# Kernel optimization log

Hardware: AMD Instinct MI355X
Metric: run time of the kernel (lower is better)

The kernel has to match this reference:

```python
import jax, jax.numpy as jnp
import numpy as np

LAYERS, STACKS = 10, 4
DILATIONS = [2 ** l for _ in range(STACKS) for l in range(LAYERS)]  # 40 blocks


def setup_inputs() -> dict:
    key = jax.random.key(0)
    ks = jax.random.split(key, 7)
    B, C, L, SC, NB = 4, 64, 8192, 256, len(DILATIONS)
    scale = 0.05  # keep 40 stacked residual blocks numerically tame
    return {
        "x": jax.random.normal(ks[0], (B, C, L), dtype=jnp.float32),
        "dc_w": jax.random.normal(ks[1], (NB, C, C, 2), dtype=jnp.float32) * scale,
        "dc_b": jax.random.normal(ks[2], (NB, C), dtype=jnp.float32) * scale,
        "conv_w": jax.random.normal(ks[3], (NB, C, C), dtype=jnp.float32) * scale,
        "conv_b": jax.random.normal(ks[4], (NB, C), dtype=jnp.float32) * scale,
        "skip_w": jax.random.normal(ks[5], (NB, SC, C), dtype=jnp.float32) * scale,
        "skip_b": jax.random.normal(ks[6], (NB, SC), dtype=jnp.float32) * scale,
        "skip_size": 4096,
    }


def reference(x, dc_w, dc_b, conv_w, conv_b, skip_w, skip_b, skip_size):
    # x: [B, res_ch, L]; returns stacked skips [n_blocks, B, skip_ch, skip_size]
    out = x
    skips = []
    for i, d in enumerate(DILATIONS):
        h = (jnp.einsum('oi,bil->bol', dc_w[i, :, :, 0], out[:, :, :-d])
             + jnp.einsum('oi,bil->bol', dc_w[i, :, :, 1], out[:, :, d:])
             + dc_b[i][None, :, None])
        g = jax.nn.relu(h)
        r = jnp.einsum('oi,bil->bol', conv_w[i], g) + conv_b[i][None, :, None]
        out = r + out[:, :, -r.shape[2]:]  # residual on aligned (last) timesteps
        s = jnp.einsum('oi,bil->bol', skip_w[i], g) + skip_b[i][None, :, None]
        skips.append(s[:, :, -skip_size:])
    return jnp.stack(skips)
```

## Files before the change

kernel.cpp:

```cpp
#include <hip/hip_runtime.h>


#define CC    64
#define SCC   256
#define BB    4
#define LL0   8192
#define NBLK  40
#define SKIPN 4096
#define TTC   32
#define STT   64

typedef __attribute__((ext_vector_type(8))) short bf16x8;
typedef __attribute__((ext_vector_type(4))) float f32x4;

__device__ __forceinline__ unsigned short f2bf(float f) {
    union { float f; unsigned u; } v; v.f = f;
    return (unsigned short)((v.u + 0x7FFF + ((v.u >> 16) & 1)) >> 16);
}

__global__ __launch_bounds__(256) void prep_weights(
    const float* __restrict__ dc_w, const float* __restrict__ conv_w,
    const float* __restrict__ skip_w,
    unsigned short* __restrict__ wcat,
    unsigned short* __restrict__ cwb,
    unsigned short* __restrict__ swb)
{
    const int n_sw = NBLK * SCC * CC;
    const int n_cw = NBLK * CC * CC;
    const int n_wc = NBLK * CC * 128;
    for (int idx = blockIdx.x * blockDim.x + threadIdx.x; idx < n_sw;
         idx += gridDim.x * blockDim.x) {
        swb[idx] = f2bf(skip_w[idx]);
        if (idx < n_cw) cwb[idx] = f2bf(conv_w[idx]);
        if (idx < n_wc) {
            const int i = idx >> 13, o = (idx >> 7) & 63, kk = idx & 127;
            wcat[idx] = f2bf(dc_w[(((i * CC + o) * CC) + (kk & 63)) * 2 + (kk >> 6)]);
        }
    }
}

__device__ __forceinline__ void skip_body(
    int id, const unsigned short* __restrict__ g,
    const unsigned short* __restrict__ sw, const float* __restrict__ sb,
    float* __restrict__ op)
{
    const int tid = threadIdx.x, lane = tid & 63, wv = tid >> 6;
    const int tt = id & 63;
    const int b  = id >> 6;
    const unsigned short* gb = g + (size_t)b * SKIPN * CC;
    float* ob = op + (size_t)b * SCC * SKIPN;

    const int trow = tt * STT + wv * 16 + (lane & 15);
    bf16x8 a[2];
    #pragma unroll
    for (int ks = 0; ks < 2; ++ks)
        a[ks] = *(const bf16x8*)(gb + (size_t)trow * CC + ks * 32 + (lane >> 4) * 8);

    const int tstore = tt * STT + wv * 16 + ((lane >> 4) << 2);
    #pragma unroll 4
    for (int n = 0; n < 16; ++n) {
        const int sc = n * 16 + (lane & 15);
        const float bias = sb[sc];
        f32x4 acc = (f32x4){bias, bias, bias, bias};
        const unsigned short* wrow = sw + sc * CC + (lane >> 4) * 8;
        acc = __builtin_amdgcn_mfma_f32_16x16x32_bf16(a[0], *(const bf16x8*)(wrow), acc, 0, 0, 0);
        acc = __builtin_amdgcn_mfma_f32_16x16x32_bf16(a[1], *(const bf16x8*)(wrow + 32), acc, 0, 0, 0);
        *(float4*)(ob + (size_t)sc * SKIPN + tstore) = (float4){acc[0], acc[1], acc[2], acc[3]};
    }
}

__global__ __launch_bounds__(256) void block_kernel(
    const float* __restrict__ cur, float* __restrict__ nxt,
    const unsigned short* __restrict__ wcat, const unsigned short* __restrict__ cwb,
    const float* __restrict__ db, const float* __restrict__ cb,
    unsigned short* __restrict__ g_out,
    int d, int Lin, int Lout, int ntiles,
    const unsigned short* __restrict__ g_prev,
    const unsigned short* __restrict__ swb_prev,
    const float* __restrict__ sb_prev,
    float* __restrict__ out_prev)
{
    const int wg = blockIdx.x;
    const int chain_wgs = BB * ntiles;
    if (wg >= chain_wgs) {
        skip_body(wg - chain_wgs, g_prev, swb_prev, sb_prev, out_prev);
        return;
    }

    __shared__ __align__(16) unsigned short xt[TTC * 128];
    __shared__ __align__(16) unsigned short gs[TTC * CC];
    __shared__ float x1f[CC][TTC + 1];

    const int tid = threadIdx.x, lane = tid & 63, wv = tid >> 6;
    const int b  = wg / ntiles;
    const int t0 = (wg % ntiles) * TTC;
    const float* src = cur + (size_t)b * CC * LL0;

    {
        const int c  = (tid & 31) * 2;
        const int tg = tid >> 5;
        const bool full = (t0 + TTC + d <= Lin);
        #pragma unroll
        for (int op = 0; op < 2; ++op) {
            const int doff = op ? d : 0;
            const int tb = t0 + tg * 4 + doff;
            float v0[4], v1[4];
            if (full && (op == 0 || (d & 3) == 0)) {
                *(float4*)v0 = *(const float4*)(src + (size_t)c * LL0 + tb);
                *(float4*)v1 = *(const float4*)(src + (size_t)(c + 1) * LL0 + tb);
            } else {
                #pragma unroll
                for (int j = 0; j < 4; ++j) {
                    int t = tb + j; if (t > Lin - 1) t = Lin - 1;
                    v0[j] = src[(size_t)c * LL0 + t];
                    v1[j] = src[(size_t)(c + 1) * LL0 + t];
                }
            }
            const int kk = op * 64 + c;
            const int chunk = kk >> 3, sub = kk & 7;
            #pragma unroll
            for (int j = 0; j < 4; ++j) {
                const int row = tg * 4 + j;
                const unsigned pack = (unsigned)f2bf(v0[j]) | ((unsigned)f2bf(v1[j]) << 16);
                *(unsigned*)((char*)xt + row * 256 + ((chunk ^ (row & 7)) * 16) + sub * 2) = pack;
            }
            if (op == 1) {
                #pragma unroll
                for (int j = 0; j < 4; ++j) {
                    x1f[c][tg * 4 + j]     = v0[j];
                    x1f[c + 1][tg * 4 + j] = v1[j];
                }
            }
        }
    }
    __syncthreads();

    const int rf = wv >> 1;
    const int oh = wv & 1;

    bf16x8 a1[4];
    {
        const int row = rf * 16 + (lane & 15);
        #pragma unroll
        for (int ks = 0; ks < 4; ++ks) {
            const int chunk = ks * 4 + (lane >> 4);
            a1[ks] = *(const bf16x8*)((const char*)xt + row * 256 + ((chunk ^ (row & 7)) * 16));
        }
    }
    f32x4 acc[2];
    #pragma unroll
    for (int n = 0; n < 2; ++n) {
        const int o = oh * 32 + n * 16 + (lane & 15);
        const float bias = db[o];
        acc[n] = (f32x4){bias, bias, bias, bias};
        const unsigned short* wrow = wcat + o * 128 + (lane >> 4) * 8;
        #pragma unroll
        for (int ks = 0; ks < 4; ++ks)
            acc[n] = __builtin_amdgcn_mfma_f32_16x16x32_bf16(
                a1[ks], *(const bf16x8*)(wrow + ks * 32), acc[n], 0, 0, 0);
    }
    {
        const int trow0 = rf * 16 + ((lane >> 4) << 2);
        #pragma unroll
        for (int n = 0; n < 2; ++n) {
            const int o = oh * 32 + n * 16 + (lane & 15);
            const int chunkb = o >> 3, sub = o & 7;
            #pragma unroll
            for (int r = 0; r < 4; ++r) {
                float g = acc[n][r]; g = g > 0.f ? g : 0.f;
                const int row = trow0 + r;
                *(unsigned short*)((char*)gs + row * 128 + ((chunkb ^ (row & 7)) * 16) + sub * 2) = f2bf(g);
            }
        }
    }
    __syncthreads();

    bf16x8 a2[2];
    {
        const int row = rf * 16 + (lane & 15);
        #pragma unroll
        for (int ks = 0; ks < 2; ++ks) {
            const int chunk = ks * 4 + (lane >> 4);
            a2[ks] = *(const bf16x8*)((const char*)gs + row * 128 + ((chunk ^ (row & 7)) * 16));
        }
    }
    {
        const int tloc = rf * 16 + ((lane >> 4) << 2);
        const int t = t0 + tloc;
        #pragma unroll
        for (int n = 0; n < 2; ++n) {
            const int o = oh * 32 + n * 16 + (lane & 15);
            const float bias = cb[o];
            f32x4 racc = (f32x4){bias, bias, bias, bias};
            const unsigned short* wrow = cwb + o * 64 + (lane >> 4) * 8;
            racc = __builtin_amdgcn_mfma_f32_16x16x32_bf16(a2[0], *(const bf16x8*)(wrow), racc, 0, 0, 0);
            racc = __builtin_amdgcn_mfma_f32_16x16x32_bf16(a2[1], *(const bf16x8*)(wrow + 32), racc, 0, 0, 0);
            float* outp = nxt + (size_t)b * CC * LL0 + (size_t)o * LL0 + t;
            if (t + 3 < Lout) {
                *(float4*)outp = (float4){racc[0] + x1f[o][tloc + 0],
                                          racc[1] + x1f[o][tloc + 1],
                                          racc[2] + x1f[o][tloc + 2],
                                          racc[3] + x1f[o][tloc + 3]};
            } else {
                #pragma unroll
                for (int r = 0; r < 4; ++r)
                    if (t + r < Lout) outp[r] = racc[r] + x1f[o][tloc + r];
            }
        }
    }

    {
        const int skip_start = Lout - SKIPN;
        const int row = tid >> 3;
        const int ch  = tid & 7;
        const int t = t0 + row;
        if (t >= skip_start && t < Lout) {
            unsigned short* gr = g_out + ((size_t)b * SKIPN + (t - skip_start)) * CC;
            bf16x8 vv = *(const bf16x8*)((const char*)gs + row * 128 + ((ch ^ (row & 7)) * 16));
            *(bf16x8*)(gr + ch * 8) = vv;
        }
    }
}

__global__ __launch_bounds__(256) void skip_kernel(
    const unsigned short* __restrict__ g, const unsigned short* __restrict__ sw,
    const float* __restrict__ sb, float* __restrict__ op)
{
    skip_body(blockIdx.x, g, sw, sb, op);
}

extern "C" void kernel_launch(void* const* d_in, const int* in_sizes, int n_in,
                              void* d_out, int out_size, void* d_ws, size_t ws_size,
                              hipStream_t stream)
{
    const float* x      = (const float*)d_in[0];
    const float* dc_w   = (const float*)d_in[1];
    const float* dc_b   = (const float*)d_in[2];
    const float* conv_w = (const float*)d_in[3];
    const float* conv_b = (const float*)d_in[4];
    const float* skip_w = (const float*)d_in[5];
    const float* skip_b = (const float*)d_in[6];
    float* out = (float*)d_out;

    char* ws = (char*)d_ws;
    float* buf0 = (float*)ws;                    ws += (size_t)BB * CC * LL0 * 4;
    float* buf1 = (float*)ws;                    ws += (size_t)BB * CC * LL0 * 4;
    unsigned short* g_all = (unsigned short*)ws; ws += (size_t)NBLK * BB * SKIPN * CC * 2;
    unsigned short* wcat  = (unsigned short*)ws; ws += (size_t)NBLK * CC * 128 * 2;
    unsigned short* cwb   = (unsigned short*)ws; ws += (size_t)NBLK * CC * CC * 2;
    unsigned short* swb   = (unsigned short*)ws; ws += (size_t)NBLK * SCC * CC * 2;

    prep_weights<<<1024, 256, 0, stream>>>(dc_w, conv_w, skip_w, wcat, cwb, swb);

    const int skip_wgs = BB * (SKIPN / STT);
    int Lc = LL0;
    for (int i = 0; i < NBLK; ++i) {
        const int d = 1 << (i % 10);
        const int Lout = Lc - d;
        const int ntiles = (Lout + TTC - 1) / TTC;
        const float* curp = (i == 0) ? x : ((i & 1) ? buf0 : buf1);
        float*       nxtp = (i & 1) ? buf1 : buf0;
        const int j = i - 1;
        const int grid = BB * ntiles + (i ? skip_wgs : 0);
        block_kernel<<<dim3(grid), 256, 0, stream>>>(
            curp, nxtp,
            wcat + (size_t)i * CC * 128, cwb + (size_t)i * CC * CC,
            dc_b + i * CC, conv_b + i * CC,
            g_all + (size_t)i * BB * SKIPN * CC,
            d, Lc, Lout, ntiles,
            g_all + (size_t)(i ? j : 0) * BB * SKIPN * CC,
            swb + (size_t)(i ? j : 0) * SCC * CC,
            skip_b + (i ? j : 0) * SCC,
            out + (size_t)(i ? j : 0) * BB * SCC * SKIPN);
        Lc = Lout;
    }
    skip_kernel<<<dim3(skip_wgs), 256, 0, stream>>>(
        g_all + (size_t)(NBLK - 1) * BB * SKIPN * CC,
        swb + (size_t)(NBLK - 1) * SCC * CC,
        skip_b + (NBLK - 1) * SCC,
        out + (size_t)(NBLK - 1) * BB * SCC * SKIPN);
}
```

Before: 853.1 us.

## Fuse small-dilation WaveNet blocks in shared memory with time-major activation layout

Activations switch from channel-major to time-major layout through a new transpose kernel. The first six blocks of each stack (dilations 1 to 32) now run in one fused kernel that keeps a haloed tile in LDS across all six layers, so the residual stream does not make global round-trips between them. The skip GEMMs for all six fused blocks overlap with the next launch. This cuts launches and global traffic for the residual stream. In exchange it recomputes the halo rows and uses larger LDS footprints with 512-thread blocks, which may reduce occupancy.

Measured after the change: 742.6 us. 1.15x faster.

```diff
diff --git a/kernel.cpp b/kernel.cpp
--- a/kernel.cpp
+++ b/kernel.cpp
@@ -8,7 +8,6 @@
 #define NBLK  40
 #define SKIPN 4096
 #define TTC   32
-#define STT   64
 
 typedef __attribute__((ext_vector_type(8))) short bf16x8;
 typedef __attribute__((ext_vector_type(4))) float f32x4;
@@ -16,6 +15,25 @@
 __device__ __forceinline__ unsigned short f2bf(float f) {
     union { float f; unsigned u; } v; v.f = f;
     return (unsigned short)((v.u + 0x7FFF + ((v.u >> 16) & 1)) >> 16);
+}
+__device__ __forceinline__ bf16x8 pack8(f32x4 u0, f32x4 u1) {
+    bf16x8 r;
+    r[0] = (short)f2bf(u0[0]); r[1] = (short)f2bf(u0[1]);
+    r[2] = (short)f2bf(u0[2]); r[3] = (short)f2bf(u0[3]);
+    r[4] = (short)f2bf(u1[0]); r[5] = (short)f2bf(u1[1]);
+    r[6] = (short)f2bf(u1[2]); r[7] = (short)f2bf(u1[3]);
+    return r;
+}
+__device__ __forceinline__ int sws(int row, int c) {
+    return (row << 6) + (((((c >> 3) ^ row) & 7) << 3) | (c & 7));
+}
+__device__ __forceinline__ int swg(int row, int o) {
+    return (row << 6) + (((((o >> 3) ^ row) & 7) << 3) | (o & 7));
+}
+__device__ __forceinline__ int swx(int row, int kk) {
+    int ch = kk >> 3;
+    ch = (ch & 8) | ((ch ^ row) & 7);
+    return (row << 7) + (ch << 3) + (kk & 7);
 }
 
 __global__ __launch_bounds__(256) void prep_weights(
@@ -39,24 +57,55 @@
     }
 }
 
+__global__ __launch_bounds__(256) void transpose_x(
+    const float* __restrict__ x, float* __restrict__ dst)
+{
+    __shared__ float tile[64][65];
+    const int b = blockIdx.y, t0 = blockIdx.x * 64;
+    const int tid = threadIdx.x;
+    #pragma unroll
+    for (int p = 0; p < 4; ++p) {
+        const int c = p * 16 + (tid >> 4);
+        const int j = tid & 15;
+        const float4 v = *(const float4*)(x + ((size_t)b * CC + c) * LL0 + t0 + j * 4);
+        tile[c][j * 4 + 0] = v.x; tile[c][j * 4 + 1] = v.y;
+        tile[c][j * 4 + 2] = v.z; tile[c][j * 4 + 3] = v.w;
+    }
+    __syncthreads();
+    #pragma unroll
+    for (int p = 0; p < 4; ++p) {
+        const int r = p * 16 + (tid >> 4);
+        const int h = tid & 15;
+        float4 v = {tile[h * 4 + 0][r], tile[h * 4 + 1][r],
+                    tile[h * 4 + 2][r], tile[h * 4 + 3][r]};
+        *(float4*)(dst + ((size_t)b * LL0 + t0 + r) * CC + h * 4) = v;
+    }
+}
+
+template<int NW>
 __device__ __forceinline__ void skip_body(
-    int id, const unsigned short* __restrict__ g,
-    const unsigned short* __restrict__ sw, const float* __restrict__ sb,
-    float* __restrict__ op)
-{
+    int e, int prev_blk0,
+    const unsigned short* __restrict__ g_all,
+    const unsigned short* __restrict__ swb,
+    const float* __restrict__ skip_b, float* __restrict__ out)
+{
+    constexpr int ROWS = NW * 16;
+    constexpr int TPB = (SKIPN / ROWS) * BB;
     const int tid = threadIdx.x, lane = tid & 63, wv = tid >> 6;
-    const int tt = id & 63;
-    const int b  = id >> 6;
-    const unsigned short* gb = g + (size_t)b * SKIPN * CC;
-    float* ob = op + (size_t)b * SCC * SKIPN;
-
-    const int trow = tt * STT + wv * 16 + (lane & 15);
+    const int j = prev_blk0 + e / TPB;
+    const int id = e % TPB;
+    const int tt = id % (SKIPN / ROWS);
+    const int b  = id / (SKIPN / ROWS);
+    const unsigned short* g = g_all + ((size_t)j * BB + b) * SKIPN * CC;
+    const unsigned short* sw = swb + (size_t)j * SCC * CC;
+    const float* sb = skip_b + j * SCC;
+    float* op = out + ((size_t)j * BB + b) * SCC * SKIPN;
+
+    const int trow = tt * ROWS + wv * 16 + (lane & 15);
     bf16x8 a[2];
-    #pragma unroll
-    for (int ks = 0; ks < 2; ++ks)
-        a[ks] = *(const bf16x8*)(gb + (size_t)trow * CC + ks * 32 + (lane >> 4) * 8);
-
-    const int tstore = tt * STT + wv * 16 + ((lane >> 4) << 2);
+    a[0] = *(const bf16x8*)(g + (size_t)trow * CC + (lane >> 4) * 8);
+    a[1] = *(const bf16x8*)(g + (size_t)trow * CC + 32 + (lane >> 4) * 8);
+    const int tstore = tt * ROWS + wv * 16 + ((lane >> 4) << 2);
     #pragma unroll 4
     for (int n = 0; n < 16; ++n) {
         const int sc = n * 16 + (lane & 15);
@@ -65,7 +114,171 @@
         const unsigned short* wrow = sw + sc * CC + (lane >> 4) * 8;
         acc = __builtin_amdgcn_mfma_f32_16x16x32_bf16(a[0], *(const bf16x8*)(wrow), acc, 0, 0, 0);
         acc = __builtin_amdgcn_mfma_f32_16x16x32_bf16(a[1], *(const bf16x8*)(wrow + 32), acc, 0, 0, 0);
-        *(float4*)(ob + (size_t)sc * SKIPN + tstore) = (float4){acc[0], acc[1], acc[2], acc[3]};
+        *(float4*)(op + (size_t)sc * SKIPN + tstore) = (float4){acc[0], acc[1], acc[2], acc[3]};
+    }
+}
+
+template<int NB, int DB, int TOUT, int R0CAP, int GSCAP, int MAXCH>
+__global__ __launch_bounds__(512) void fused_kernel(
+    const float* __restrict__ cur, float* __restrict__ nxt,
+    const unsigned short* __restrict__ wcat_all, const unsigned short* __restrict__ cwb_all,
+    const float* __restrict__ db_all, const float* __restrict__ cb_all,
+    unsigned short* __restrict__ g_all, int blk0, int Lin, int ntiles,
+    const unsigned short* __restrict__ swb, const float* __restrict__ skip_b,
+    float* __restrict__ out, int prev_blk0, int prev_nblk)
+{
+    const int wg = blockIdx.x;
+    const int chain = BB * ntiles;
+    if (wg >= chain) {
+        skip_body<8>(wg - chain, prev_blk0, g_all, swb, skip_b, out);
+        return;
+    }
+
+    constexpr int H  = DB * ((1 << NB) - 1);
+    constexpr int R0 = TOUT + H;
+    __shared__ __align__(16) float sm[R0CAP * CC];
+    __shared__ __align__(16) unsigned short gsm[GSCAP * CC];
+
+    const int tid = threadIdx.x, lane = tid & 63, wv = tid >> 6;
+    const int b = wg / ntiles, t0 = (wg % ntiles) * TOUT;
+    const float* src = cur + (size_t)b * LL0 * CC;
+
+    for (int base = 0; base < R0; base += 32) {
+        const int row = base + (tid >> 4);
+        const int h = tid & 15;
+        if (row < R0) {
+            int gt = t0 + row; if (gt > Lin - 1) gt = Lin - 1;
+            *(f32x4*)(sm + sws(row, h * 4)) =
+                *(const f32x4*)(src + (size_t)gt * CC + h * 4);
+        }
+    }
+    __syncthreads();
+
+    const int rf = wv >> 1, oh = wv & 1;
+    int Rcur = R0, Lj = Lin;
+
+    for (int j = 0; j < NB; ++j) {
+        const int d = DB << j;
+        const int Rn = Rcur - d;
+        Lj -= d;
+        const unsigned short* wj  = wcat_all + (size_t)(blk0 + j) * CC * 128;
+        const unsigned short* cj  = cwb_all + (size_t)(blk0 + j) * CC * CC;
+        const float* dbj = db_all + (blk0 + j) * CC;
+        const float* cbj = cb_all + (blk0 + j) * CC;
+
+        #pragma unroll
+        for (int ch = 0; ch < MAXCH; ++ch) {
+            if (ch * 64 < Rn) {
+                int row = ch * 64 + rf * 16 + (lane & 15);
+                if (row > Rn - 1) row = Rn - 1;
+                bf16x8 a1[4];
+                #pragma unroll
+                for (int ks = 0; ks < 2; ++ks) {
+                    const int c0 = ks * 32 + (lane >> 4) * 8;
+                    a1[ks] = pack8(*(const f32x4*)(sm + sws(row, c0)),
+                                   *(const f32x4*)(sm + sws(row, c0 + 4)));
+                    a1[2 + ks] = pack8(*(const f32x4*)(sm + sws(row + d, c0)),
+                                       *(const f32x4*)(sm + sws(row + d, c0 + 4)));
+                }
+                f32x4 acc[2];
+                #pragma unroll
+                for (int n = 0; n < 2; ++n) {
+                    const int o = oh * 32 + n * 16 + (lane & 15);
+                    const float bias = dbj[o];
+                    acc[n] = (f32x4){bias, bias, bias, bias};
+                    const unsigned short* wrow = wj + o * 128 + (lane >> 4) * 8;
+                    #pragma unroll
+                    for (int ks = 0; ks < 4; ++ks)
+                        acc[n] = __builtin_amdgcn_mfma_f32_16x16x32_bf16(
+                            a1[ks], *(const bf16x8*)(wrow + ks * 32), acc[n], 0, 0, 0);
+                }
+                const int wr = ch * 64 + rf * 16 + ((lane >> 4) << 2);
+                #pragma unroll
+                for (int n = 0; n < 2; ++n) {
+                    const int o = oh * 32 + n * 16 + (lane & 15);
+                    #pragma unroll
+                    for (int r = 0; r < 4; ++r) {
+                        const int rr = wr + r;
+                        if (rr < Rn) {
+                            float g = acc[n][r]; g = g > 0.f ? g : 0.f;
+                            gsm[swg(rr, o)] = f2bf(g);
+                        }
+                    }
+                }
+            }
+        }
+        __syncthreads();
+
+        f32x4 racc[MAXCH][2];
+        f32x4 oldv[MAXCH][2];
+        #pragma unroll
+        for (int ch = 0; ch < MAXCH; ++ch) {
+            if (ch * 64 < Rn) {
+                int row = ch * 64 + rf * 16 + (lane & 15);
+                if (row > Rn - 1) row = Rn - 1;
+                bf16x8 a2[2];
+                #pragma unroll
+                for (int ks = 0; ks < 2; ++ks)
+                    a2[ks] = *(const bf16x8*)(gsm + swg(row, ks * 32 + (lane >> 4) * 8));
+                const int wr = ch * 64 + rf * 16 + ((lane >> 4) << 2);
+                #pragma unroll
+                for (int n = 0; n < 2; ++n) {
+                    const int o = oh * 32 + n * 16 + (lane & 15);
+                    const float bias = cbj[o];
+                    racc[ch][n] = (f32x4){bias, bias, bias, bias};
+                    const unsigned short* wrow = cj + o * CC + (lane >> 4) * 8;
+                    racc[ch][n] = __builtin_amdgcn_mfma_f32_16x16x32_bf16(
+                        a2[0], *(const bf16x8*)(wrow), racc[ch][n], 0, 0, 0);
+                    racc[ch][n] = __builtin_amdgcn_mfma_f32_16x16x32_bf16(
+                        a2[1], *(const bf16x8*)(wrow + 32), racc[ch][n], 0, 0, 0);
+                    #pragma unroll
+                    for (int r = 0; r < 4; ++r) {
+                        int rr = wr + r; if (rr > Rn - 1) rr = Rn - 1;
+                        oldv[ch][n][r] = sm[sws(rr + d, o)];
+                    }
+                }
+            }
+        }
+        __syncthreads();
+
+        #pragma unroll
+        for (int ch = 0; ch < MAXCH; ++ch) {
+            if (ch * 64 < Rn) {
+                const int wr = ch * 64 + rf * 16 + ((lane >> 4) << 2);
+                #pragma unroll
+                for (int n = 0; n < 2; ++n) {
+                    const int o = oh * 32 + n * 16 + (lane & 15);
+                    #pragma unroll
+                    for (int r = 0; r < 4; ++r) {
+                        const int rr = wr + r;
+                        if (rr < Rn) sm[sws(rr, o)] = racc[ch][n][r] + oldv[ch][n][r];
+                    }
+                }
+            }
+        }
+        {
+            const int wbase = Lj - SKIPN;
+            unsigned short* gdst = g_all + ((size_t)(blk0 + j) * BB + b) * SKIPN * CC;
+            const int ch8 = tid & 7;
+            for (int grow = tid >> 3; grow < Rn; grow += 64) {
+                const int gt = t0 + grow;
+                if (gt < Lj && gt >= wbase)
+                    *(bf16x8*)(gdst + ((size_t)(gt - wbase)) * CC + ch8 * 8) =
+                        *(const bf16x8*)(gsm + (grow << 6) + (((ch8 ^ grow) & 7) << 3));
+            }
+        }
+        __syncthreads();
+        Rcur = Rn;
+    }
+
+    float* dst = nxt + (size_t)b * LL0 * CC;
+    for (int base = 0; base < TOUT; base += 32) {
+        const int row = base + (tid >> 4);
+        const int h = tid & 15;
+        const int gt = t0 + row;
+        if (row < TOUT && gt < Lj)
+            *(float4*)(dst + (size_t)gt * CC + h * 4) =
+                *(const float4*)(sm + sws(row, h * 4));
     }
 }
 
@@ -75,78 +288,55 @@
     const float* __restrict__ db, const float* __restrict__ cb,
     unsigned short* __restrict__ g_out,
     int d, int Lin, int Lout, int ntiles,
-    const unsigned short* __restrict__ g_prev,
-    const unsigned short* __restrict__ swb_prev,
-    const float* __restrict__ sb_prev,
-    float* __restrict__ out_prev)
+    const unsigned short* __restrict__ g_all, const unsigned short* __restrict__ swb,
+    const float* __restrict__ skip_b, float* __restrict__ out,
+    int prev_blk0, int prev_nblk)
 {
     const int wg = blockIdx.x;
-    const int chain_wgs = BB * ntiles;
-    if (wg >= chain_wgs) {
-        skip_body(wg - chain_wgs, g_prev, swb_prev, sb_prev, out_prev);
+    const int chain = BB * ntiles;
+    if (wg >= chain) {
+        skip_body<4>(wg - chain, prev_blk0, g_all, swb, skip_b, out);
         return;
     }
 
     __shared__ __align__(16) unsigned short xt[TTC * 128];
     __shared__ __align__(16) unsigned short gs[TTC * CC];
     __shared__ float x1f[CC][TTC + 1];
+    __shared__ __align__(16) float rs[TTC * CC];
 
     const int tid = threadIdx.x, lane = tid & 63, wv = tid >> 6;
-    const int b  = wg / ntiles;
-    const int t0 = (wg % ntiles) * TTC;
-    const float* src = cur + (size_t)b * CC * LL0;
-
-    {
-        const int c  = (tid & 31) * 2;
-        const int tg = tid >> 5;
-        const bool full = (t0 + TTC + d <= Lin);
-        #pragma unroll
-        for (int op = 0; op < 2; ++op) {
-            const int doff = op ? d : 0;
-            const int tb = t0 + tg * 4 + doff;
-            float v0[4], v1[4];
-            if (full && (op == 0 || (d & 3) == 0)) {
-                *(float4*)v0 = *(const float4*)(src + (size_t)c * LL0 + tb);
-                *(float4*)v1 = *(const float4*)(src + (size_t)(c + 1) * LL0 + tb);
-            } else {
-                #pragma unroll
-                for (int j = 0; j < 4; ++j) {
-                    int t = tb + j; if (t > Lin - 1) t = Lin - 1;
-                    v0[j] = src[(size_t)c * LL0 + t];
-                    v1[j] = src[(size_t)(c + 1) * LL0 + t];
-                }
-            }
-            const int kk = op * 64 + c;
-            const int chunk = kk >> 3, sub = kk & 7;
-            #pragma unroll
-            for (int j = 0; j < 4; ++j) {
-                const int row = tg * 4 + j;
-                const unsigned pack = (unsigned)f2bf(v0[j]) | ((unsigned)f2bf(v1[j]) << 16);
-                *(unsigned*)((char*)xt + row * 256 + ((chunk ^ (row & 7)) * 16) + sub * 2) = pack;
-            }
-            if (op == 1) {
-                #pragma unroll
-                for (int j = 0; j < 4; ++j) {
-                    x1f[c][tg * 4 + j]     = v0[j];
-                    x1f[c + 1][tg * 4 + j] = v1[j];
-                }
-            }
-        }
+    const int b = wg / ntiles, t0 = (wg % ntiles) * TTC;
+    const float* src = cur + (size_t)b * LL0 * CC;
+
+    #pragma unroll
+    for (int p = 0; p < 2; ++p) {
+        const int row = p * 16 + (tid >> 4);
+        const int h = tid & 15;
+        int ta = t0 + row;     if (ta > Lin - 1) ta = Lin - 1;
+        int tb = t0 + row + d; if (tb > Lin - 1) tb = Lin - 1;
+        const float4 v0 = *(const float4*)(src + (size_t)ta * CC + h * 4);
+        const float4 v1 = *(const float4*)(src + (size_t)tb * CC + h * 4);
+        uint2 p0, p1;
+        p0.x = (unsigned)f2bf(v0.x) | ((unsigned)f2bf(v0.y) << 16);
+        p0.y = (unsigned)f2bf(v0.z) | ((unsigned)f2bf(v0.w) << 16);
+        p1.x = (unsigned)f2bf(v1.x) | ((unsigned)f2bf(v1.y) << 16);
+        p1.y = (unsigned)f2bf(v1.z) | ((unsigned)f2bf(v1.w) << 16);
+        *(uint2*)(xt + swx(row, h * 4)) = p0;
+        *(uint2*)(xt + swx(row, 64 + h * 4)) = p1;
+        x1f[h * 4 + 0][row] = v1.x;
+        x1f[h * 4 + 1][row] = v1.y;
+        x1f[h * 4 + 2][row] = v1.z;
+        x1f[h * 4 + 3][row] = v1.w;
     }
     __syncthreads();
 
-    const int rf = wv >> 1;
-    const int oh = wv & 1;
+    const int rf = wv >> 1, oh = wv & 1;
+    const int row = rf * 16 + (lane & 15);
 
     bf16x8 a1[4];
-    {
-        const int row = rf * 16 + (lane & 15);
-        #pragma unroll
-        for (int ks = 0; ks < 4; ++ks) {
-            const int chunk = ks * 4 + (lane >> 4);
-            a1[ks] = *(const bf16x8*)((const char*)xt + row * 256 + ((chunk ^ (row & 7)) * 16));
-        }
-    }
+    #pragma unroll
+    for (int ks = 0; ks < 4; ++ks)
+        a1[ks] = *(const bf16x8*)(xt + swx(row, ks * 32 + (lane >> 4) * 8));
     f32x4 acc[2];
     #pragma unroll
     for (int n = 0; n < 2; ++n) {
@@ -159,74 +349,60 @@
             acc[n] = __builtin_amdgcn_mfma_f32_16x16x32_bf16(
                 a1[ks], *(const bf16x8*)(wrow + ks * 32), acc[n], 0, 0, 0);
     }
+    const int wr = rf * 16 + ((lane >> 4) << 2);
+    #pragma unroll
+    for (int n = 0; n < 2; ++n) {
+        const int o = oh * 32 + n * 16 + (lane & 15);
+        #pragma unroll
+        for (int r = 0; r < 4; ++r) {
+            float g = acc[n][r]; g = g > 0.f ? g : 0.f;
+            gs[swg(wr + r, o)] = f2bf(g);
+        }
+    }
+    __syncthreads();
+
+    bf16x8 a2[2];
+    #pragma unroll
+    for (int ks = 0; ks < 2; ++ks)
+        a2[ks] = *(const bf16x8*)(gs + swg(row, ks * 32 + (lane >> 4) * 8));
+    #pragma unroll
+    for (int n = 0; n < 2; ++n) {
+        const int o = oh * 32 + n * 16 + (lane & 15);
+        const float bias = cb[o];
+        f32x4 racc = (f32x4){bias, bias, bias, bias};
+        const unsigned short* wrow = cwb + o * CC + (lane >> 4) * 8;
+        racc = __builtin_amdgcn_mfma_f32_16x16x32_bf16(a2[0], *(const bf16x8*)(wrow), racc, 0, 0, 0);
+        racc = __builtin_amdgcn_mfma_f32_16x16x32_bf16(a2[1], *(const bf16x8*)(wrow + 32), racc, 0, 0, 0);
+        #pragma unroll
+        for (int r = 0; r < 4; ++r)
+            rs[sws(wr + r, o)] = racc[r] + x1f[o][wr + r];
+    }
+    __syncthreads();
+
+    #pragma unroll
+    for (int p = 0; p < 2; ++p) {
+        const int row2 = p * 16 + (tid >> 4);
+        const int h = tid & 15;
+        const int t = t0 + row2;
+        if (t < Lout)
+            *(float4*)(nxt + (size_t)b * LL0 * CC + (size_t)t * CC + h * 4) =
+                *(const float4*)(rs + sws(row2, h * 4));
+    }
     {
-        const int trow0 = rf * 16 + ((lane >> 4) << 2);
-        #pragma unroll
-        for (int n = 0; n < 2; ++n) {
-            const int o = oh * 32 + n * 16 + (lane & 15);
-            const int chunkb = o >> 3, sub = o & 7;
-            #pragma unroll
-            for (int r = 0; r < 4; ++r) {
-                float g = acc[n][r]; g = g > 0.f ? g : 0.f;
-                const int row = trow0 + r;
-                *(unsigned short*)((char*)gs + row * 128 + ((chunkb ^ (row & 7)) * 16) + sub * 2) = f2bf(g);
-            }
-        }
-    }
-    __syncthreads();
-
-    bf16x8 a2[2];
-    {
-        const int row = rf * 16 + (lane & 15);
-        #pragma unroll
-        for (int ks = 0; ks < 2; ++ks) {
-            const int chunk = ks * 4 + (lane >> 4);
-            a2[ks] = *(const bf16x8*)((const char*)gs + row * 128 + ((chunk ^ (row & 7)) * 16));
-        }
-    }
-    {
-        const int tloc = rf * 16 + ((lane >> 4) << 2);
-        const int t = t0 + tloc;
-        #pragma unroll
-        for (int n = 0; n < 2; ++n) {
-            const int o = oh * 32 + n * 16 + (lane & 15);
-            const float bias = cb[o];
-            f32x4 racc = (f32x4){bias, bias, bias, bias};
-            const unsigned short* wrow = cwb + o * 64 + (lane >> 4) * 8;
-            racc = __builtin_amdgcn_mfma_f32_16x16x32_bf16(a2[0], *(const bf16x8*)(wrow), racc, 0, 0, 0);
-            racc = __builtin_amdgcn_mfma_f32_16x16x32_bf16(a2[1], *(const bf16x8*)(wrow + 32), racc, 0, 0, 0);
-            float* outp = nxt + (size_t)b * CC * LL0 + (size_t)o * LL0 + t;
-            if (t + 3 < Lout) {
-                *(float4*)outp = (float4){racc[0] + x1f[o][tloc + 0],
-                                          racc[1] + x1f[o][tloc + 1],
-                                          racc[2] + x1f[o][tloc + 2],
-                                          racc[3] + x1f[o][tloc + 3]};
-            } else {
-                #pragma unroll
-                for (int r = 0; r < 4; ++r)
-                    if (t + r < Lout) outp[r] = racc[r] + x1f[o][tloc + r];
-            }
-        }
-    }
-
-    {
-        const int skip_start = Lout - SKIPN;
-        const int row = tid >> 3;
-        const int ch  = tid & 7;
-        const int t = t0 + row;
-        if (t >= skip_start && t < Lout) {
-            unsigned short* gr = g_out + ((size_t)b * SKIPN + (t - skip_start)) * CC;
-            bf16x8 vv = *(const bf16x8*)((const char*)gs + row * 128 + ((ch ^ (row & 7)) * 16));
-            *(bf16x8*)(gr + ch * 8) = vv;
-        }
+        const int row2 = tid >> 3, ch8 = tid & 7;
+        const int t = t0 + row2;
+        const int wbase = Lout - SKIPN;
+        if (t >= wbase && t < Lout)
+            *(bf16x8*)(g_out + ((size_t)b * SKIPN + (t - wbase)) * CC + ch8 * 8) =
+                *(const bf16x8*)(gs + (row2 << 6) + (((ch8 ^ row2) & 7) << 3));
     }
 }
 
 __global__ __launch_bounds__(256) void skip_kernel(
-    const unsigned short* __restrict__ g, const unsigned short* __restrict__ sw,
-    const float* __restrict__ sb, float* __restrict__ op)
-{
-    skip_body(blockIdx.x, g, sw, sb, op);
+    const unsigned short* __restrict__ g_all, const unsigned short* __restrict__ swb,
+    const float* __restrict__ skip_b, float* __restrict__ out, int blk)
+{
+    skip_body<4>(blockIdx.x, blk, g_all, swb, skip_b, out);
 }
 
 extern "C" void kernel_launch(void* const* d_in, const int* in_sizes, int n_in,
@@ -243,40 +419,43 @@
     float* out = (float*)d_out;
 
     char* ws = (char*)d_ws;
-    float* buf0 = (float*)ws;                    ws += (size_t)BB * CC * LL0 * 4;
-    float* buf1 = (float*)ws;                    ws += (size_t)BB * CC * LL0 * 4;
+    float* bufA = (float*)ws;                    ws += (size_t)BB * LL0 * CC * 4;
+    float* bufB = (float*)ws;                    ws += (size_t)BB * LL0 * CC * 4;
     unsigned short* g_all = (unsigned short*)ws; ws += (size_t)NBLK * BB * SKIPN * CC * 2;
     unsigned short* wcat  = (unsigned short*)ws; ws += (size_t)NBLK * CC * 128 * 2;
     unsigned short* cwb   = (unsigned short*)ws; ws += (size_t)NBLK * CC * CC * 2;
     unsigned short* swb   = (unsigned short*)ws; ws += (size_t)NBLK * SCC * CC * 2;
 
     prep_weights<<<1024, 256, 0, stream>>>(dc_w, conv_w, skip_w, wcat, cwb, swb);
-
-    const int skip_wgs = BB * (SKIPN / STT);
-    int Lc = LL0;
-    for (int i = 0; i < NBLK; ++i) {
-        const int d = 1 << (i % 10);
-        const int Lout = Lc - d;
-        const int ntiles = (Lout + TTC - 1) / TTC;
-        const float* curp = (i == 0) ? x : ((i & 1) ? buf0 : buf1);
-        float*       nxtp = (i & 1) ? buf1 : buf0;
-        const int j = i - 1;
-        const int grid = BB * ntiles + (i ? skip_wgs : 0);
-        block_kernel<<<dim3(grid), 256, 0, stream>>>(
-            curp, nxtp,
-            wcat + (size_t)i * CC * 128, cwb + (size_t)i * CC * CC,
-            dc_b + i * CC, conv_b + i * CC,
-            g_all + (size_t)i * BB * SKIPN * CC,
-            d, Lc, Lout, ntiles,
-            g_all + (size_t)(i ? j : 0) * BB * SKIPN * CC,
-            swb + (size_t)(i ? j : 0) * SCC * CC,
-            skip_b + (i ? j : 0) * SCC,
-            out + (size_t)(i ? j : 0) * BB * SCC * SKIPN);
-        Lc = Lout;
-    }
-    skip_kernel<<<dim3(skip_wgs), 256, 0, stream>>>(
-        g_all + (size_t)(NBLK - 1) * BB * SKIPN * CC,
-        swb + (size_t)(NBLK - 1) * SCC * CC,
-        skip_b + (NBLK - 1) * SCC,
-        out + (size_t)(NBLK - 1) * BB * SCC * SKIPN);
-}
+    transpose_x<<<dim3(LL0 / 64, BB), 256, 0, stream>>>(x, bufA);
+
+    float* bufs[2] = {bufA, bufB};
+    int Lc = LL0, blk = 0, q = 0, pb0 = 0, pnb = 0;
+    for (int s = 0; s < 4; ++s) {
+        {
+            const int Lout = Lc - 63;
+            const int nt = (Lout + 95) / 96;
+            const int grid = BB * nt + pnb * 128;
+            fused_kernel<6, 1, 96, 160, 160, 3><<<dim3(grid), 512, 0, stream>>>(
+                bufs[q & 1], bufs[(q + 1) & 1], wcat, cwb, dc_b, conv_b,
+                g_all, blk, Lc, nt, swb, skip_b, out, pb0, pnb);
+            pb0 = blk; pnb = 6; blk += 6; Lc = Lout; ++q;
+        }
+        for (int dl = 6; dl < 10; ++dl) {
+            const int d = 1 << dl;
+            const int Lout = Lc - d;
+            const int nt = (Lout + TTC - 1) / TTC;
+            const int grid = BB * nt + pnb * 256;
+            block_kernel<<<dim3(grid), 256, 0, stream>>>(
+                bufs[q & 1], bufs[(q + 1) & 1],
+                wcat + (size_t)blk * CC * 128, cwb + (size_t)blk * CC * CC,
+                dc_b + blk * CC, conv_b + blk * CC,
+                g_all + (size_t)blk * BB * SKIPN * CC,
+                d, Lc, Lout, nt,
+                g_all, swb, skip_b, out, pb0, pnb);
+            pb0 = blk; pnb = 1; blk += 1; Lc = Lout; ++q;
+        }
+    }
+    skip_kernel<<<dim3(BB * (SKIPN / 64)), 256, 0, stream>>>(
+        g_all, swb, skip_b, out, NBLK - 1);
+}
```
